# Kernel tuning notes

Hardware: AMD Instinct MI355X
Metric: run time of the kernel (lower is better)

Reference implementation:

```python
import jax, jax.numpy as jnp
import numpy as np

# Inner-product factors for Cl(1,3) (Minkowski metric diag(+,-,-,-)).
# For blade e_b, <~e_b e_b>_0 = product of the metric signs of its constituent vectors.
# Blade order: [1, e0,e1,e2,e3, e01,e02,e03,e12,e13,e23, e012,e013,e023,e123, e0123]
_IPF = jnp.array([1, 1, -1, -1, -1, -1, -1, -1, 1, 1, 1, 1, 1, 1, -1, -1], dtype=jnp.float32)

B, H, N, CMV, CS = 4, 8, 2048, 8, 16


def setup_inputs() -> dict:
    key = jax.random.key(0)
    ks = jax.random.split(key, 6)
    f = lambda k, s: jax.random.normal(k, s, dtype=jnp.float32)
    return {
        "q_mv": f(ks[0], (B, H, N, CMV, 16)),
        "k_mv": f(ks[1], (B, H, N, CMV, 16)),
        "v_mv": f(ks[2], (B, H, N, CMV, 16)),
        "q_s": f(ks[3], (B, H, N, CS)),
        "k_s": f(ks[4], (B, H, N, CS)),
        "v_s": f(ks[5], (B, H, N, CS)),
    }


def reference(q_mv, k_mv, v_mv, q_s, k_s, v_s):
    b, h, n, cmv, _ = q_mv.shape
    cs = q_s.shape[-1]
    cmv_out = v_mv.shape[-2]
    cs_out = v_s.shape[-1]
    # GA inner product on mv part = euclidean dot after applying metric factors to queries
    q = jnp.concatenate([(q_mv * _IPF).reshape(b, h, n, cmv * 16), q_s], axis=-1)
    k = jnp.concatenate([k_mv.reshape(b, h, n, cmv * 16), k_s], axis=-1)
    v = jnp.concatenate([v_mv.reshape(b, h, n, cmv_out * 16), v_s], axis=-1)
    scale = 1.0 / np.sqrt(q.shape[-1]).astype(np.float32)  # torch SDPA default scale
    scores = jnp.einsum("bhid,bhjd->bhij", q, k) * scale  # [B,H,N,N]
    attn = jax.nn.softmax(scores, axis=-1)
    out = jnp.einsum("bhij,bhjd->bhid", attn, v)
    out_mv = out[..., : cmv_out * 16].reshape(b, h, n, cmv_out, 16)
    out_s = out[..., cmv_out * 16 : cmv_out * 16 + cs_out]
    return out_mv, out_s
```

## Files before the change

kernel.cpp:

```cpp
#include <hip/hip_runtime.h>
#include <cstdint>
#include <math.h>


#define BH    32
#define N_    2048
#define DMV   128
#define DS    16
#define D_    144
#define BM    256
#define BN    64
#define NKIT  (N_ / BN)
#define KSTR  152
#define VSTR  72
#define SVROWS 160
#define KCHUNKS (BN * KSTR / 8)
#define VCHUNKS (D_ * VSTR / 8)
#define KP_BYTES ((size_t)BH * N_ * KSTR * 2)
#define QSCALE 0.12022458674074693f
#define KPACK_BLOCKS (BH * N_ * 19 / 256)
#define TSTR  156

typedef __bf16 bf16_8 __attribute__((ext_vector_type(8)));
typedef __bf16 bf16_4 __attribute__((ext_vector_type(4)));
typedef __bf16 bf16_2 __attribute__((ext_vector_type(2)));
typedef float  f32x4  __attribute__((ext_vector_type(4)));
typedef float  f32x16 __attribute__((ext_vector_type(16)));

#define GLOAD_LDS16(g, l)                                                     \
  __builtin_amdgcn_global_load_lds(                                           \
      (const __attribute__((address_space(1))) void*)(g),                     \
      (__attribute__((address_space(3))) void*)(l), 16, 0, 0)

__device__ __forceinline__ f32x16 mfma32(bf16_8 a, bf16_8 b, f32x16 c) {
  return __builtin_amdgcn_mfma_f32_32x32x16_bf16(a, b, c, 0, 0, 0);
}

__device__ __forceinline__ bf16_4 cvt4(f32x4 x) {
  bf16_4 w; w[0]=(__bf16)x[0]; w[1]=(__bf16)x[1]; w[2]=(__bf16)x[2]; w[3]=(__bf16)x[3];
  return w;
}

__global__ __launch_bounds__(256)
void pack_kv(const float* __restrict__ kmv, const float* __restrict__ ks_,
             const float* __restrict__ vmv, const float* __restrict__ vs,
             __bf16* __restrict__ kp, __bf16* __restrict__ vt) {
  __shared__ __align__(16) __bf16 sT[64 * TSTR];
  const int t = threadIdx.x;
  const int b = blockIdx.x;
  if (b < KPACK_BLOCKS) {
    const unsigned g = b * 256u + t;
    const unsigned row = g / 19u, seg = g - row * 19u;
    bf16_8 o;
    if (seg < 16) {
      const f32x4* p = (const f32x4*)(kmv + (size_t)row * DMV + seg * 8);
      f32x4 a = p[0], bb = p[1];
#pragma unroll
      for (int j = 0; j < 8; ++j) o[j] = (__bf16)((j < 4) ? a[j] : bb[j - 4]);
    } else if (seg < 18) {
      const f32x4* p = (const f32x4*)(ks_ + (size_t)row * DS + (seg - 16) * 8);
      f32x4 a = p[0], bb = p[1];
#pragma unroll
      for (int j = 0; j < 8; ++j) o[j] = (__bf16)((j < 4) ? a[j] : bb[j - 4]);
    } else {
#pragma unroll
      for (int j = 0; j < 8; ++j) o[j] = (__bf16)0.0f;
    }
    *(bf16_8*)(kp + (size_t)row * KSTR + seg * 8) = o;
    return;
  }
  const int tile = b - KPACK_BLOCKS;
  const int n = t >> 2, c = t & 3;
  const float* mv = vmv + (size_t)(tile * 64 + n) * DMV;
  const float* sv = vs  + (size_t)(tile * 64 + n) * DS;
  __bf16* row = &sT[n * TSTR];
  if (c < 3) {
#pragma unroll
    for (int i = 0; i < 9; ++i)
      *(bf16_4*)&row[c * 36 + 4 * i] = cvt4(*(const f32x4*)(mv + c * 36 + 4 * i));
  } else {
#pragma unroll
    for (int i = 0; i < 5; ++i)
      *(bf16_4*)&row[108 + 4 * i] = cvt4(*(const f32x4*)(mv + 108 + 4 * i));
#pragma unroll
    for (int i = 0; i < 4; ++i)
      *(bf16_4*)&row[128 + 4 * i] = cvt4(*(const f32x4*)(sv + 4 * i));
  }
  __syncthreads();
  __bf16* vtt = vt + (size_t)tile * (D_ * VSTR);
#pragma unroll
  for (int k = 0; k < 18; ++k) {
    int idx = t + 256 * k;
    int d = idx >> 5, j = idx & 31;
    bf16_2 p; p[0] = sT[(2 * j) * TSTR + d]; p[1] = sT[(2 * j + 1) * TSTR + d];
    *(bf16_2*)&vtt[d * VSTR + 2 * j] = p;
  }
}

__device__ __forceinline__ bf16_8 load_q_frag(const float* qmv_row, const float* qs_row, int k0) {
  bf16_8 f;
  if (k0 < DMV) {
    const f32x4* p = (const f32x4*)(qmv_row + k0);
    f32x4 a = p[0], b = p[1];
    int hi8 = k0 & 8;
#pragma unroll
    for (int j = 0; j < 8; ++j) {
      float v = (j < 4) ? a[j] : b[j - 4];
      bool pos = hi8 ? (j < 6) : (j < 2);
      f[j] = (__bf16)(v * (pos ? QSCALE : -QSCALE));
    }
  } else {
    const f32x4* p = (const f32x4*)(qs_row + (k0 - DMV));
    f32x4 a = p[0], b = p[1];
#pragma unroll
    for (int j = 0; j < 8; ++j) {
      float v = (j < 4) ? a[j] : b[j - 4];
      f[j] = (__bf16)(v * QSCALE);
    }
  }
  return f;
}

__global__ __launch_bounds__(512, 2)
void geo_attn_kernel(const float* __restrict__ q_mv, const float* __restrict__ q_s,
                     const __bf16* __restrict__ kp, const __bf16* __restrict__ vt,
                     float* __restrict__ out)
{
  __shared__ __align__(16) __bf16 sK[2][BN * KSTR];
  __shared__ __align__(16) __bf16 sVT[2][SVROWS * VSTR];

  const int tid  = threadIdx.x;
  const int w    = tid >> 6;
  const int lane = tid & 63;
  const int c32  = lane & 31;
  const int hi   = lane >> 5;
  const int flat = blockIdx.x;
  const int xcd  = flat & 7;
  const int jj   = flat >> 3;
  const int bh   = xcd * 4 + (jj & 3);
  const int qb   = jj >> 2;
  const int qbase = qb * BM;
  const size_t bh_n = (size_t)bh * N_;

  if (tid < 288) {
    int bb = tid / 144, cc = tid - bb * 144;
    f32x4 z = {0.f, 0.f, 0.f, 0.f};
    *(f32x4*)((char*)&sVT[bb][D_ * VSTR] + cc * 16) = z;
  }

  bf16_8 qf[9];
  {
    const int mrow = qbase + w * 32 + c32;
    const float* qmv_row = q_mv + (bh_n + mrow) * DMV;
    const float* qs_row  = q_s  + (bh_n + mrow) * DS;
#pragma unroll
    for (int ks = 0; ks < 9; ++ks)
      qf[ks] = load_q_frag(qmv_row, qs_row, ks * 16 + hi * 8);
  }

  f32x16 of[5];
#pragma unroll
  for (int dt = 0; dt < 5; ++dt)
#pragma unroll
    for (int r = 0; r < 16; ++r) of[dt][r] = 0.0f;
  float m_i = -INFINITY, l_i = 0.0f;

  const __bf16* kbase = kp + bh_n * KSTR;
  const __bf16* vbase = vt + (size_t)bh * NKIT * (D_ * VSTR);

  auto stage = [&](int it, int bu) {
    const __bf16* kt  = kbase + (size_t)(it * BN) * KSTR;
    const __bf16* vtt = vbase + (size_t)it * (D_ * VSTR);
    __bf16* dK = &sK[bu][0];
    __bf16* dV = &sVT[bu][0];
#pragma unroll
    for (int s = 0; s < 2; ++s)
      GLOAD_LDS16(kt + (tid + 512 * s) * 8, dK + (tid + 512 * s) * 8);
    if (tid < KCHUNKS - 1024)
      GLOAD_LDS16(kt + (tid + 1024) * 8, dK + (tid + 1024) * 8);
#pragma unroll
    for (int s = 0; s < 2; ++s)
      GLOAD_LDS16(vtt + (tid + 512 * s) * 8, dV + (tid + 512 * s) * 8);
    if (tid < VCHUNKS - 1024)
      GLOAD_LDS16(vtt + (tid + 1024) * 8, dV + (tid + 1024) * 8);
  };

  stage(0, 0);
  __syncthreads();

  for (int it = 0; it < NKIT; ++it) {
    const int cur = it & 1;
    if (it + 1 < NKIT) stage(it + 1, cur ^ 1);

    f32x16 sf[2];
#pragma unroll
    for (int nt = 0; nt < 2; ++nt)
#pragma unroll
      for (int r = 0; r < 16; ++r) sf[nt][r] = 0.0f;
    __builtin_amdgcn_s_setprio(1);
#pragma unroll
    for (int ks = 0; ks < 9; ++ks) {
      bf16_8 kb0 = *(const bf16_8*)&sK[cur][(c32)      * KSTR + ks * 16 + hi * 8];
      bf16_8 kb1 = *(const bf16_8*)&sK[cur][(32 + c32) * KSTR + ks * 16 + hi * 8];
      sf[0] = mfma32(kb0, qf[ks], sf[0]);
      sf[1] = mfma32(kb1, qf[ks], sf[1]);
    }
    __builtin_amdgcn_s_setprio(0);

    float al = 1.0f, m_use;
    {
      float mx = sf[0][0];
#pragma unroll
      for (int r = 1; r < 16; ++r) mx = fmaxf(mx, sf[0][r]);
#pragma unroll
      for (int r = 0; r < 16; ++r) mx = fmaxf(mx, sf[1][r]);
      mx = fmaxf(mx, __shfl_xor(mx, 32));

      if (__all(mx <= m_i + 8.0f)) {
        m_use = m_i;
      } else {
        float mnew = fmaxf(m_i, mx);
        al = __builtin_amdgcn_exp2f(m_i - mnew);
        m_i = mnew; m_use = mnew;
#pragma unroll
        for (int r = 0; r < 16; ++r) {
          float a = __shfl(al, (r & 3) + 8 * (r >> 2) + 4 * hi);
#pragma unroll
          for (int dt = 0; dt < 5; ++dt) of[dt][r] *= a;
        }
      }
      float rs = 0.0f;
#pragma unroll
      for (int nt = 0; nt < 2; ++nt)
#pragma unroll
        for (int r = 0; r < 16; ++r) {
          float p = __builtin_amdgcn_exp2f(sf[nt][r] - m_use);
          sf[nt][r] = p;
          rs += p;
        }
      rs += __shfl_xor(rs, 32);
      l_i = l_i * al + rs;
    }

#pragma unroll
    for (int ks = 0; ks < 4; ++ks) {
      const int nt = ks >> 1;
      const int Ra = 8 * (ks & 1);
      unsigned x0, x1, y0, y1;
      asm("v_cvt_pk_bf16_f32 %0, %1, %2" : "=v"(x0) : "v"(sf[nt][Ra + 0]), "v"(sf[nt][Ra + 1]));
      asm("v_cvt_pk_bf16_f32 %0, %1, %2" : "=v"(x1) : "v"(sf[nt][Ra + 2]), "v"(sf[nt][Ra + 3]));
      asm("v_cvt_pk_bf16_f32 %0, %1, %2" : "=v"(y0) : "v"(sf[nt][Ra + 4]), "v"(sf[nt][Ra + 5]));
      asm("v_cvt_pk_bf16_f32 %0, %1, %2" : "=v"(y1) : "v"(sf[nt][Ra + 6]), "v"(sf[nt][Ra + 7]));
      auto s0 = __builtin_amdgcn_permlane32_swap(x0, y0, false, false);
      auto s1 = __builtin_amdgcn_permlane32_swap(x1, y1, false, false);
      union { unsigned u[4]; bf16_8 v; } pu;
      pu.u[0] = s0[0]; pu.u[1] = s1[0]; pu.u[2] = s0[1]; pu.u[3] = s1[1];
      __builtin_amdgcn_s_setprio(1);
#pragma unroll
      for (int dt = 0; dt < 5; ++dt) {
        bf16_8 vb = *(const bf16_8*)&sVT[cur][(dt * 32 + c32) * VSTR + ks * 16 + hi * 8];
        of[dt] = mfma32(pu.v, vb, of[dt]);
      }
      __builtin_amdgcn_s_setprio(0);
    }
    __syncthreads();
  }

  float* out_mv = out;
  float* out_s  = out + (size_t)BH * N_ * DMV;
#pragma unroll
  for (int r = 0; r < 16; ++r) {
    const int ml  = (r & 3) + 8 * (r >> 2) + 4 * hi;
    const float linv = __builtin_amdgcn_rcpf(__shfl(l_i, ml));
    const int row = qbase + w * 32 + ml;
#pragma unroll
    for (int dt = 0; dt < 4; ++dt)
      out_mv[(bh_n + row) * DMV + dt * 32 + c32] = of[dt][r] * linv;
    if (c32 < DS)
      out_s[(bh_n + row) * DS + c32] = of[4][r] * linv;
  }
}

extern "C" void kernel_launch(void* const* d_in, const int* in_sizes, int n_in,
                              void* d_out, int out_size, void* d_ws, size_t ws_size,
                              hipStream_t stream) {
  (void)in_sizes; (void)n_in; (void)out_size; (void)ws_size;
  const float* q_mv = (const float*)d_in[0];
  const float* k_mv = (const float*)d_in[1];
  const float* v_mv = (const float*)d_in[2];
  const float* q_s  = (const float*)d_in[3];
  const float* k_s  = (const float*)d_in[4];
  const float* v_s  = (const float*)d_in[5];
  float* out = (float*)d_out;

  __bf16* kp = (__bf16*)d_ws;
  __bf16* vt = (__bf16*)((char*)d_ws + KP_BYTES);

  pack_kv<<<KPACK_BLOCKS + BH * NKIT, 256, 0, stream>>>(k_mv, k_s, v_mv, v_s, kp, vt);

  geo_attn_kernel<<<dim3(256), 512, 0, stream>>>(q_mv, q_s, kp, vt, out);
}
```

Baseline: 239.5 us.

## Load V fragments directly from global into registers instead of LDS

```diff
diff --git a/kernel.cpp b/kernel.cpp
--- a/kernel.cpp
+++ b/kernel.cpp
@@ -12,18 +12,15 @@
 #define BN    64
 #define NKIT  (N_ / BN)
 #define KSTR  152
-#define VSTR  72
-#define SVROWS 160
 #define KCHUNKS (BN * KSTR / 8)
-#define VCHUNKS (D_ * VSTR / 8)
 #define KP_BYTES ((size_t)BH * N_ * KSTR * 2)
+#define VT_CHUNKS 1152
 #define QSCALE 0.12022458674074693f
 #define KPACK_BLOCKS (BH * N_ * 19 / 256)
 #define TSTR  156
 
 typedef __bf16 bf16_8 __attribute__((ext_vector_type(8)));
 typedef __bf16 bf16_4 __attribute__((ext_vector_type(4)));
-typedef __bf16 bf16_2 __attribute__((ext_vector_type(2)));
 typedef float  f32x4  __attribute__((ext_vector_type(4)));
 typedef float  f32x16 __attribute__((ext_vector_type(16)));
 
@@ -87,13 +84,17 @@
       *(bf16_4*)&row[128 + 4 * i] = cvt4(*(const f32x4*)(sv + 4 * i));
   }
   __syncthreads();
-  __bf16* vtt = vt + (size_t)tile * (D_ * VSTR);
-#pragma unroll
-  for (int k = 0; k < 18; ++k) {
-    int idx = t + 256 * k;
-    int d = idx >> 5, j = idx & 31;
-    bf16_2 p; p[0] = sT[(2 * j) * TSTR + d]; p[1] = sT[(2 * j + 1) * TSTR + d];
-    *(bf16_2*)&vtt[d * VSTR + 2 * j] = p;
+  bf16_8* vtt = (bf16_8*)vt + (size_t)tile * VT_CHUNKS;
+#pragma unroll
+  for (int s = 0; s < 5; ++s) {
+    int cc = t + 256 * s;
+    if (cc < VT_CHUNKS) {
+      int g = cc / 144, d = cc - g * 144;
+      bf16_8 o;
+#pragma unroll
+      for (int j = 0; j < 8; ++j) o[j] = sT[(g * 8 + j) * TSTR + d];
+      vtt[cc] = o;
+    }
   }
 }
 
@@ -127,7 +128,6 @@
                      float* __restrict__ out)
 {
   __shared__ __align__(16) __bf16 sK[2][BN * KSTR];
-  __shared__ __align__(16) __bf16 sVT[2][SVROWS * VSTR];
 
   const int tid  = threadIdx.x;
   const int w    = tid >> 6;
@@ -142,12 +142,6 @@
   const int qbase = qb * BM;
   const size_t bh_n = (size_t)bh * N_;
 
-  if (tid < 288) {
-    int bb = tid / 144, cc = tid - bb * 144;
-    f32x4 z = {0.f, 0.f, 0.f, 0.f};
-    *(f32x4*)((char*)&sVT[bb][D_ * VSTR] + cc * 16) = z;
-  }
-
   bf16_8 qf[9];
   {
     const int mrow = qbase + w * 32 + c32;
@@ -166,23 +160,16 @@
   float m_i = -INFINITY, l_i = 0.0f;
 
   const __bf16* kbase = kp + bh_n * KSTR;
-  const __bf16* vbase = vt + (size_t)bh * NKIT * (D_ * VSTR);
+  const bf16_8* vbase = (const bf16_8*)vt + (size_t)bh * NKIT * VT_CHUNKS;
 
   auto stage = [&](int it, int bu) {
-    const __bf16* kt  = kbase + (size_t)(it * BN) * KSTR;
-    const __bf16* vtt = vbase + (size_t)it * (D_ * VSTR);
+    const __bf16* kt = kbase + (size_t)(it * BN) * KSTR;
     __bf16* dK = &sK[bu][0];
-    __bf16* dV = &sVT[bu][0];
 #pragma unroll
     for (int s = 0; s < 2; ++s)
       GLOAD_LDS16(kt + (tid + 512 * s) * 8, dK + (tid + 512 * s) * 8);
     if (tid < KCHUNKS - 1024)
       GLOAD_LDS16(kt + (tid + 1024) * 8, dK + (tid + 1024) * 8);
-#pragma unroll
-    for (int s = 0; s < 2; ++s)
-      GLOAD_LDS16(vtt + (tid + 512 * s) * 8, dV + (tid + 512 * s) * 8);
-    if (tid < VCHUNKS - 1024)
-      GLOAD_LDS16(vtt + (tid + 1024) * 8, dV + (tid + 1024) * 8);
   };
 
   stage(0, 0);
@@ -190,6 +177,17 @@
 
   for (int it = 0; it < NKIT; ++it) {
     const int cur = it & 1;
+
+    bf16_8 vf[4][5];
+    {
+      const bf16_8* vtile = vbase + (size_t)it * VT_CHUNKS + (hi * 144 + c32);
+#pragma unroll
+      for (int ks = 0; ks < 4; ++ks)
+#pragma unroll
+        for (int dt = 0; dt < 5; ++dt)
+          vf[ks][dt] = vtile[ks * 288 + dt * 32];
+    }
+
     if (it + 1 < NKIT) stage(it + 1, cur ^ 1);
 
     f32x16 sf[2];
@@ -257,10 +255,8 @@
       pu.u[0] = s0[0]; pu.u[1] = s1[0]; pu.u[2] = s0[1]; pu.u[3] = s1[1];
       __builtin_amdgcn_s_setprio(1);
 #pragma unroll
-      for (int dt = 0; dt < 5; ++dt) {
-        bf16_8 vb = *(const bf16_8*)&sVT[cur][(dt * 32 + c32) * VSTR + ks * 16 + hi * 8];
-        of[dt] = mfma32(pu.v, vb, of[dt]);
-      }
+      for (int dt = 0; dt < 5; ++dt)
+        of[dt] = mfma32(pu.v, vf[ks][dt], of[dt]);
       __builtin_amdgcn_s_setprio(0);
     }
     __syncthreads();
```

New measurement: 249.3 us. 1.04x slower.

## Software-pipeline QK^T of next tile with softmax/PV of current tile

Applied to the files above, without the earlier changes.

```diff
diff --git a/kernel.cpp b/kernel.cpp
--- a/kernel.cpp
+++ b/kernel.cpp
@@ -127,11 +127,11 @@
                      float* __restrict__ out)
 {
   __shared__ __align__(16) __bf16 sK[2][BN * KSTR];
-  __shared__ __align__(16) __bf16 sVT[2][SVROWS * VSTR];
+  __shared__ __align__(16) __bf16 sVT[3][SVROWS * VSTR];
 
   const int tid  = threadIdx.x;
+  const int lane = tid & 63;
   const int w    = tid >> 6;
-  const int lane = tid & 63;
   const int c32  = lane & 31;
   const int hi   = lane >> 5;
   const int flat = blockIdx.x;
@@ -142,7 +142,7 @@
   const int qbase = qb * BM;
   const size_t bh_n = (size_t)bh * N_;
 
-  if (tid < 288) {
+  if (tid < 432) {
     int bb = tid / 144, cc = tid - bb * 144;
     f32x4 z = {0.f, 0.f, 0.f, 0.f};
     *(f32x4*)((char*)&sVT[bb][D_ * VSTR] + cc * 16) = z;
@@ -168,52 +168,56 @@
   const __bf16* kbase = kp + bh_n * KSTR;
   const __bf16* vbase = vt + (size_t)bh * NKIT * (D_ * VSTR);
 
-  auto stage = [&](int it, int bu) {
-    const __bf16* kt  = kbase + (size_t)(it * BN) * KSTR;
-    const __bf16* vtt = vbase + (size_t)it * (D_ * VSTR);
+  auto stageK = [&](int it, int bu) {
+    const __bf16* kt = kbase + (size_t)(it * BN) * KSTR;
     __bf16* dK = &sK[bu][0];
-    __bf16* dV = &sVT[bu][0];
-#pragma unroll
-    for (int s = 0; s < 2; ++s)
-      GLOAD_LDS16(kt + (tid + 512 * s) * 8, dK + (tid + 512 * s) * 8);
+    GLOAD_LDS16(kt + tid * 8, dK + tid * 8);
+    GLOAD_LDS16(kt + (tid + 512) * 8, dK + (tid + 512) * 8);
     if (tid < KCHUNKS - 1024)
       GLOAD_LDS16(kt + (tid + 1024) * 8, dK + (tid + 1024) * 8);
-#pragma unroll
-    for (int s = 0; s < 2; ++s)
-      GLOAD_LDS16(vtt + (tid + 512 * s) * 8, dV + (tid + 512 * s) * 8);
+  };
+  auto stageV = [&](int it, int bu) {
+    const __bf16* vtt = vbase + (size_t)it * (D_ * VSTR);
+    __bf16* dV = &sVT[bu][0];
+    GLOAD_LDS16(vtt + tid * 8, dV + tid * 8);
+    GLOAD_LDS16(vtt + (tid + 512) * 8, dV + (tid + 512) * 8);
     if (tid < VCHUNKS - 1024)
       GLOAD_LDS16(vtt + (tid + 1024) * 8, dV + (tid + 1024) * 8);
   };
 
-  stage(0, 0);
-  __syncthreads();
-
-  for (int it = 0; it < NKIT; ++it) {
-    const int cur = it & 1;
-    if (it + 1 < NKIT) stage(it + 1, cur ^ 1);
-
-    f32x16 sf[2];
+  auto qk = [&](int kb, f32x16 (&sn)[2]) {
 #pragma unroll
     for (int nt = 0; nt < 2; ++nt)
 #pragma unroll
-      for (int r = 0; r < 16; ++r) sf[nt][r] = 0.0f;
+      for (int r = 0; r < 16; ++r) sn[nt][r] = 0.0f;
     __builtin_amdgcn_s_setprio(1);
 #pragma unroll
     for (int ks = 0; ks < 9; ++ks) {
-      bf16_8 kb0 = *(const bf16_8*)&sK[cur][(c32)      * KSTR + ks * 16 + hi * 8];
-      bf16_8 kb1 = *(const bf16_8*)&sK[cur][(32 + c32) * KSTR + ks * 16 + hi * 8];
-      sf[0] = mfma32(kb0, qf[ks], sf[0]);
-      sf[1] = mfma32(kb1, qf[ks], sf[1]);
+      bf16_8 kb0 = *(const bf16_8*)&sK[kb][(c32)      * KSTR + ks * 16 + hi * 8];
+      bf16_8 kb1 = *(const bf16_8*)&sK[kb][(32 + c32) * KSTR + ks * 16 + hi * 8];
+      sn[0] = mfma32(kb0, qf[ks], sn[0]);
+      sn[1] = mfma32(kb1, qf[ks], sn[1]);
     }
     __builtin_amdgcn_s_setprio(0);
+  };
+
+  auto body = [&](int t, f32x16 (&sfc)[2], f32x16 (&sfn)[2]) {
+    __syncthreads();
+    if (t + 2 < NKIT) {
+      stageK(t + 2, t & 1);
+      stageV(t + 2, (t + 2) % 3);
+    }
+    if (t + 1 < NKIT)
+      qk((t + 1) & 1, sfn);
 
     float al = 1.0f, m_use;
     {
-      float mx = sf[0][0];
-#pragma unroll
-      for (int r = 1; r < 16; ++r) mx = fmaxf(mx, sf[0][r]);
-#pragma unroll
-      for (int r = 0; r < 16; ++r) mx = fmaxf(mx, sf[1][r]);
+      float a[8];
+#pragma unroll
+      for (int r = 0; r < 8; ++r)
+        a[r] = fmaxf(fmaxf(sfc[0][r], sfc[0][r + 8]), fmaxf(sfc[1][r], sfc[1][r + 8]));
+      float mx = fmaxf(fmaxf(fmaxf(a[0], a[1]), fmaxf(a[2], a[3])),
+                       fmaxf(fmaxf(a[4], a[5]), fmaxf(a[6], a[7])));
       mx = fmaxf(mx, __shfl_xor(mx, 32));
 
       if (__all(mx <= m_i + 8.0f)) {
@@ -224,33 +228,35 @@
         m_i = mnew; m_use = mnew;
 #pragma unroll
         for (int r = 0; r < 16; ++r) {
-          float a = __shfl(al, (r & 3) + 8 * (r >> 2) + 4 * hi);
-#pragma unroll
-          for (int dt = 0; dt < 5; ++dt) of[dt][r] *= a;
+          float aa = __shfl(al, (r & 3) + 8 * (r >> 2) + 4 * hi);
+#pragma unroll
+          for (int dt = 0; dt < 5; ++dt) of[dt][r] *= aa;
         }
       }
-      float rs = 0.0f;
 #pragma unroll
       for (int nt = 0; nt < 2; ++nt)
 #pragma unroll
-        for (int r = 0; r < 16; ++r) {
-          float p = __builtin_amdgcn_exp2f(sf[nt][r] - m_use);
-          sf[nt][r] = p;
-          rs += p;
-        }
+        for (int r = 0; r < 16; ++r)
+          sfc[nt][r] = __builtin_amdgcn_exp2f(sfc[nt][r] - m_use);
+      float s8[8];
+#pragma unroll
+      for (int r = 0; r < 8; ++r)
+        s8[r] = (sfc[0][r] + sfc[0][r + 8]) + (sfc[1][r] + sfc[1][r + 8]);
+      float rs = ((s8[0] + s8[1]) + (s8[2] + s8[3])) + ((s8[4] + s8[5]) + (s8[6] + s8[7]));
       rs += __shfl_xor(rs, 32);
       l_i = l_i * al + rs;
     }
 
+    const __bf16* sV = &sVT[t % 3][0];
 #pragma unroll
     for (int ks = 0; ks < 4; ++ks) {
       const int nt = ks >> 1;
       const int Ra = 8 * (ks & 1);
       unsigned x0, x1, y0, y1;
-      asm("v_cvt_pk_bf16_f32 %0, %1, %2" : "=v"(x0) : "v"(sf[nt][Ra + 0]), "v"(sf[nt][Ra + 1]));
-      asm("v_cvt_pk_bf16_f32 %0, %1, %2" : "=v"(x1) : "v"(sf[nt][Ra + 2]), "v"(sf[nt][Ra + 3]));
-      asm("v_cvt_pk_bf16_f32 %0, %1, %2" : "=v"(y0) : "v"(sf[nt][Ra + 4]), "v"(sf[nt][Ra + 5]));
-      asm("v_cvt_pk_bf16_f32 %0, %1, %2" : "=v"(y1) : "v"(sf[nt][Ra + 6]), "v"(sf[nt][Ra + 7]));
+      asm("v_cvt_pk_bf16_f32 %0, %1, %2" : "=v"(x0) : "v"(sfc[nt][Ra + 0]), "v"(sfc[nt][Ra + 1]));
+      asm("v_cvt_pk_bf16_f32 %0, %1, %2" : "=v"(x1) : "v"(sfc[nt][Ra + 2]), "v"(sfc[nt][Ra + 3]));
+      asm("v_cvt_pk_bf16_f32 %0, %1, %2" : "=v"(y0) : "v"(sfc[nt][Ra + 4]), "v"(sfc[nt][Ra + 5]));
+      asm("v_cvt_pk_bf16_f32 %0, %1, %2" : "=v"(y1) : "v"(sfc[nt][Ra + 6]), "v"(sfc[nt][Ra + 7]));
       auto s0 = __builtin_amdgcn_permlane32_swap(x0, y0, false, false);
       auto s1 = __builtin_amdgcn_permlane32_swap(x1, y1, false, false);
       union { unsigned u[4]; bf16_8 v; } pu;
@@ -258,12 +264,22 @@
       __builtin_amdgcn_s_setprio(1);
 #pragma unroll
       for (int dt = 0; dt < 5; ++dt) {
-        bf16_8 vb = *(const bf16_8*)&sVT[cur][(dt * 32 + c32) * VSTR + ks * 16 + hi * 8];
+        bf16_8 vb = *(const bf16_8*)&sV[(dt * 32 + c32) * VSTR + ks * 16 + hi * 8];
         of[dt] = mfma32(pu.v, vb, of[dt]);
       }
       __builtin_amdgcn_s_setprio(0);
     }
-    __syncthreads();
+  };
+
+  f32x16 sfA[2], sfB[2];
+  stageK(0, 0); stageV(0, 0);
+  __syncthreads();
+  qk(0, sfA);
+  stageK(1, 1); stageV(1, 1);
+
+  for (int t2 = 0; t2 < NKIT; t2 += 2) {
+    body(t2,     sfA, sfB);
+    body(t2 + 1, sfB, sfA);
   }
 
   float* out_mv = out;
```

New measurement: 241.9 us. About the same (+1.0%).
